# Performance work log

Measured on AMD Instinct MI355X. Metric: run time of the kernel, lower is better.

Reference implementation:

```python
import math
import jax, jax.numpy as jnp
import numpy as np

B, N, D = 4, 4096, 1024
H, M = 16, 64
HD = D // H  # 64
EPS = 1e-6


def favor_features(data, proj):
    # data: [B,H,N,hd], proj: [M,hd] -> [B,H,N,M]
    hd = data.shape[-1]
    m = proj.shape[0]
    dn = data / math.sqrt(hd)
    norm_sq = 0.5 * jnp.sum(dn * dn, axis=-1, keepdims=True)  # [B,H,N,1]
    comb = jnp.einsum('bhnd,md->bhnm', dn, proj) - norm_sq
    comb = comb - jnp.max(comb, axis=-1, keepdims=True)
    return jnp.exp(comb) / math.sqrt(m) + EPS


def setup_inputs() -> dict:
    key = jax.random.key(0)
    ks = jax.random.split(key, 6)
    x = jax.random.normal(ks[0], (B, N, D), dtype=jnp.float32)
    qkv_w = jax.random.normal(ks[1], (3 * D, D), dtype=jnp.float32) * (1.0 / math.sqrt(D))
    qkv_b = jnp.zeros((3 * D,), dtype=jnp.float32)
    proj_w = jax.random.normal(ks[2], (D, D), dtype=jnp.float32) * (1.0 / math.sqrt(D))
    proj_b = jnp.zeros((D,), dtype=jnp.float32)
    pm = jax.random.normal(ks[3], (M, HD), dtype=jnp.float32)
    pm = pm / jnp.linalg.norm(pm, axis=-1, keepdims=True)
    return {"x": x, "qkv_w": qkv_w, "qkv_b": qkv_b, "proj_w": proj_w,
            "proj_b": proj_b, "projection_matrix": pm}


def reference(x, qkv_w, qkv_b, proj_w, proj_b, projection_matrix):
    b, n, d = x.shape
    qkv = x @ qkv_w.T + qkv_b                      # [B,N,3D]
    qkv = qkv.reshape(b, n, 3, H, HD)
    qkv = jnp.transpose(qkv, (2, 0, 3, 1, 4))      # [3,B,H,N,hd]
    q, k, v = qkv[0], qkv[1], qkv[2]
    q_p = favor_features(q, projection_matrix)     # [B,H,N,M]
    k_p = favor_features(k, projection_matrix)     # [B,H,N,M]
    kv = jnp.einsum('bhnm,bhnv->bhmv', k_p, v)     # [B,H,M,hd]
    out = jnp.einsum('bhnm,bhmv->bhnv', q_p, kv)   # [B,H,N,hd]
    k_sum = jnp.sum(k_p, axis=2)                   # [B,H,M]
    normalizer = jnp.einsum('bhnm,bhm->bhn', q_p, k_sum)[..., None]
    out = out / (normalizer + EPS)
    out = jnp.transpose(out, (0, 2, 1, 3)).reshape(b, n, d)
    return out @ proj_w.T + proj_b
```

## Files before the change

kernel.cpp:

```cpp
#include <hip/hip_runtime.h>
#include <math.h>

#define B_  4
#define N_  4096
#define D_  1024
#define H_  16
#define HD_ 64
#define M_  64
#define TD_ 3072
#define EPS_ 1e-6f

typedef __attribute__((ext_vector_type(8))) short short8;
typedef __attribute__((ext_vector_type(4))) float floatx4;
typedef unsigned int uint32;

__device__ __forceinline__ void cvt2(float f0, float f1, uint32& hp, uint32& lp)
{
    uint32 b0 = __float_as_uint(f0), b1 = __float_as_uint(f1);
    hp = (b1 & 0xFFFF0000u) | (b0 >> 16);
    float l0 = f0 - __uint_as_float(b0 & 0xFFFF0000u);
    float l1 = f1 - __uint_as_float(b1 & 0xFFFF0000u);
    lp = (__float_as_uint(l1) & 0xFFFF0000u) | (__float_as_uint(l0) >> 16);
}

#define LDSTR 40

__global__ __launch_bounds__(256, 2) void gemm_bf16x2_nt_bias(
    const float* __restrict__ A, const float* __restrict__ Bm,
    const float* __restrict__ bias, float* __restrict__ C,
    int Nx, int Kx)
{
    __shared__ __align__(16) unsigned short AhiS[128*LDSTR], AloS[128*LDSTR];
    __shared__ __align__(16) unsigned short BhiS[128*LDSTR], BloS[128*LDSTR];

    const int t    = threadIdx.x;
    const int bm   = blockIdx.y * 128, bn = blockIdx.x * 128;
    const int lane = t & 63, wave = t >> 6;
    const int wm   = wave >> 1, wn = wave & 1;
    const int l16  = lane & 15, quad = lane >> 4;
    const int r    = t >> 1;
    const int ko   = (t & 1) * 16;

    floatx4 acc[4][4];
#pragma unroll
    for (int i = 0; i < 4; i++)
#pragma unroll
        for (int j = 0; j < 4; j++) acc[i][j] = (floatx4)0.f;

    const float* ap = A  + (size_t)(bm + r) * Kx + ko;
    const float* bp = Bm + (size_t)(bn + r) * Kx + ko;

    for (int k0 = 0; k0 < Kx; k0 += 32) {
        float4 fa0 = *(const float4*)(ap + k0);
        float4 fa1 = *(const float4*)(ap + k0 + 4);
        float4 fa2 = *(const float4*)(ap + k0 + 8);
        float4 fa3 = *(const float4*)(ap + k0 + 12);
        float4 fb0 = *(const float4*)(bp + k0);
        float4 fb1 = *(const float4*)(bp + k0 + 4);
        float4 fb2 = *(const float4*)(bp + k0 + 8);
        float4 fb3 = *(const float4*)(bp + k0 + 12);

        __syncthreads();

        uint4 h0, h1, l0, l1;
        cvt2(fa0.x, fa0.y, h0.x, l0.x); cvt2(fa0.z, fa0.w, h0.y, l0.y);
        cvt2(fa1.x, fa1.y, h0.z, l0.z); cvt2(fa1.z, fa1.w, h0.w, l0.w);
        cvt2(fa2.x, fa2.y, h1.x, l1.x); cvt2(fa2.z, fa2.w, h1.y, l1.y);
        cvt2(fa3.x, fa3.y, h1.z, l1.z); cvt2(fa3.z, fa3.w, h1.w, l1.w);
        *(uint4*)&AhiS[r*LDSTR + ko]     = h0;
        *(uint4*)&AhiS[r*LDSTR + ko + 8] = h1;
        *(uint4*)&AloS[r*LDSTR + ko]     = l0;
        *(uint4*)&AloS[r*LDSTR + ko + 8] = l1;

        cvt2(fb0.x, fb0.y, h0.x, l0.x); cvt2(fb0.z, fb0.w, h0.y, l0.y);
        cvt2(fb1.x, fb1.y, h0.z, l0.z); cvt2(fb1.z, fb1.w, h0.w, l0.w);
        cvt2(fb2.x, fb2.y, h1.x, l1.x); cvt2(fb2.z, fb2.w, h1.y, l1.y);
        cvt2(fb3.x, fb3.y, h1.z, l1.z); cvt2(fb3.z, fb3.w, h1.w, l1.w);
        *(uint4*)&BhiS[r*LDSTR + ko]     = h0;
        *(uint4*)&BhiS[r*LDSTR + ko + 8] = h1;
        *(uint4*)&BloS[r*LDSTR + ko]     = l0;
        *(uint4*)&BloS[r*LDSTR + ko + 8] = l1;

        __syncthreads();

        short8 ah[4], al[4], bh[4], bl[4];
#pragma unroll
        for (int mi = 0; mi < 4; mi++) {
            int row = (wm*64 + mi*16 + l16) * LDSTR + quad*8;
            ah[mi] = *(const short8*)&AhiS[row];
            al[mi] = *(const short8*)&AloS[row];
        }
#pragma unroll
        for (int ni = 0; ni < 4; ni++) {
            int row = (wn*64 + ni*16 + l16) * LDSTR + quad*8;
            bh[ni] = *(const short8*)&BhiS[row];
            bl[ni] = *(const short8*)&BloS[row];
        }
#pragma unroll
        for (int mi = 0; mi < 4; mi++)
#pragma unroll
            for (int ni = 0; ni < 4; ni++) {
                floatx4 d = acc[mi][ni];
                d = __builtin_amdgcn_mfma_f32_16x16x32_bf16(ah[mi], bh[ni], d, 0, 0, 0);
                d = __builtin_amdgcn_mfma_f32_16x16x32_bf16(al[mi], bh[ni], d, 0, 0, 0);
                d = __builtin_amdgcn_mfma_f32_16x16x32_bf16(ah[mi], bl[ni], d, 0, 0, 0);
                acc[mi][ni] = d;
            }
    }

    float bia[4];
#pragma unroll
    for (int ni = 0; ni < 4; ni++)
        bia[ni] = bias[bn + wn*64 + ni*16 + l16];
#pragma unroll
    for (int mi = 0; mi < 4; mi++)
#pragma unroll
        for (int rr = 0; rr < 4; rr++) {
            int row = bm + wm*64 + mi*16 + quad*4 + rr;
            float* crow = C + (size_t)row * Nx + bn + wn*64 + l16;
#pragma unroll
            for (int ni = 0; ni < 4; ni++)
                crow[ni*16] = acc[mi][ni][rr] + bia[ni];
        }
}

__global__ __launch_bounds__(256) void favor_features_kernel(
    const float* __restrict__ qkvb, const float* __restrict__ proj,
    float* __restrict__ qp, float* __restrict__ kp)
{
    __shared__ float  projT[64*64];
    __shared__ float4 dnbuf[4][64];
    const int t = threadIdx.x;
    const int wave = t >> 6, lane = t & 63;
    const int part = blockIdx.y;
    float* outp = (part == 0) ? qp : kp;

    for (int i = t; i < 4096; i += 256)
        projT[(i & 63) * 64 + (i >> 6)] = proj[i];
    __syncthreads();

    const int h = blockIdx.x >> 6;
    const int n0 = (blockIdx.x & 63) * 64;
    const float* src = qkvb + part * D_ + h * HD_ + lane;

    for (int iter = 0; iter < 4; iter++) {
        const int n = n0 + iter * 16 + wave * 4;
        float v0 = src[(size_t)(n+0) * TD_];
        float v1 = src[(size_t)(n+1) * TD_];
        float v2 = src[(size_t)(n+2) * TD_];
        float v3 = src[(size_t)(n+3) * TD_];
        float4 dn = make_float4(v0*0.125f, v1*0.125f, v2*0.125f, v3*0.125f);
        dnbuf[wave][lane] = dn;
        float s0 = dn.x*dn.x, s1 = dn.y*dn.y, s2 = dn.z*dn.z, s3 = dn.w*dn.w;
#pragma unroll
        for (int off = 32; off >= 1; off >>= 1) {
            s0 += __shfl_xor(s0, off, 64);
            s1 += __shfl_xor(s1, off, 64);
            s2 += __shfl_xor(s2, off, 64);
            s3 += __shfl_xor(s3, off, 64);
        }
        float c0 = -0.5f*s0, c1 = -0.5f*s1, c2 = -0.5f*s2, c3 = -0.5f*s3;
#pragma unroll
        for (int d = 0; d < 64; d++) {
            float p = projT[d*64 + lane];
            float4 q = dnbuf[wave][d];
            c0 = fmaf(q.x, p, c0);
            c1 = fmaf(q.y, p, c1);
            c2 = fmaf(q.z, p, c2);
            c3 = fmaf(q.w, p, c3);
        }
        float m0 = c0, m1 = c1, m2 = c2, m3 = c3;
#pragma unroll
        for (int off = 32; off >= 1; off >>= 1) {
            m0 = fmaxf(m0, __shfl_xor(m0, off, 64));
            m1 = fmaxf(m1, __shfl_xor(m1, off, 64));
            m2 = fmaxf(m2, __shfl_xor(m2, off, 64));
            m3 = fmaxf(m3, __shfl_xor(m3, off, 64));
        }
        float r0 = expf(c0 - m0) * 0.125f + EPS_;
        float r1 = expf(c1 - m1) * 0.125f + EPS_;
        float r2 = expf(c2 - m2) * 0.125f + EPS_;
        float r3 = expf(c3 - m3) * 0.125f + EPS_;
        size_t orow = ((size_t)h * N_ + n) * 64 + lane;
        outp[orow]       = r0;
        outp[orow + 64]  = r1;
        outp[orow + 128] = r2;
        outp[orow + 192] = r3;
    }
}

__global__ __launch_bounds__(256) void kv_partial_kernel(
    const float* __restrict__ qkvb, const float* __restrict__ kp,
    float* __restrict__ kvpart, float* __restrict__ kspart)
{
    const int t = threadIdx.x;
    const int h = blockIdx.x;
    const int c = blockIdx.y;
    const int n0 = c * 128;
    const int m0 = (t & 15) * 4;
    const int v0 = (t >> 4) * 4;

    const float* kpsrc = kp + ((size_t)h * N_ + n0) * 64 + m0;
    const float* vsrc  = qkvb + (size_t)n0 * TD_ + 2 * D_ + h * HD_ + v0;

    float acc[4][4];
#pragma unroll
    for (int i = 0; i < 4; i++)
#pragma unroll
        for (int j = 0; j < 4; j++) acc[i][j] = 0.f;
    float ks[4] = {0.f, 0.f, 0.f, 0.f};

#pragma unroll 4
    for (int n = 0; n < 128; n++) {
        float4 kq = *(const float4*)(kpsrc + (size_t)n * 64);
        float4 vq = *(const float4*)(vsrc  + (size_t)n * TD_);
        acc[0][0] = fmaf(kq.x, vq.x, acc[0][0]);
        acc[0][1] = fmaf(kq.x, vq.y, acc[0][1]);
        acc[0][2] = fmaf(kq.x, vq.z, acc[0][2]);
        acc[0][3] = fmaf(kq.x, vq.w, acc[0][3]);
        acc[1][0] = fmaf(kq.y, vq.x, acc[1][0]);
        acc[1][1] = fmaf(kq.y, vq.y, acc[1][1]);
        acc[1][2] = fmaf(kq.y, vq.z, acc[1][2]);
        acc[1][3] = fmaf(kq.y, vq.w, acc[1][3]);
        acc[2][0] = fmaf(kq.z, vq.x, acc[2][0]);
        acc[2][1] = fmaf(kq.z, vq.y, acc[2][1]);
        acc[2][2] = fmaf(kq.z, vq.z, acc[2][2]);
        acc[2][3] = fmaf(kq.z, vq.w, acc[2][3]);
        acc[3][0] = fmaf(kq.w, vq.x, acc[3][0]);
        acc[3][1] = fmaf(kq.w, vq.y, acc[3][1]);
        acc[3][2] = fmaf(kq.w, vq.z, acc[3][2]);
        acc[3][3] = fmaf(kq.w, vq.w, acc[3][3]);
        if (v0 == 0) {
            ks[0] += kq.x; ks[1] += kq.y; ks[2] += kq.z; ks[3] += kq.w;
        }
    }

    float* kvp = kvpart + (((size_t)h * 32 + c) * 4096) + m0 * 64 + v0;
#pragma unroll
    for (int i = 0; i < 4; i++)
        *(float4*)(kvp + i * 64) = make_float4(acc[i][0], acc[i][1], acc[i][2], acc[i][3]);

    if (v0 == 0) {
        float* ksp = kspart + ((size_t)h * 32 + c) * 64 + m0;
        *(float4*)ksp = make_float4(ks[0], ks[1], ks[2], ks[3]);
    }
}

__global__ __launch_bounds__(256) void kv_reduce_kernel(
    const float* __restrict__ kvpart, const float* __restrict__ kspart,
    float* __restrict__ kv, float* __restrict__ ksum)
{
    const int t = threadIdx.x;
    const int h = blockIdx.x;
    const int e0 = t * 16;

    float4 s[4];
#pragma unroll
    for (int i = 0; i < 4; i++) s[i] = make_float4(0.f, 0.f, 0.f, 0.f);
    float kss = 0.f;

    for (int c = 0; c < 32; c++) {
        const float* p = kvpart + (((size_t)h * 32 + c) * 4096) + e0;
#pragma unroll
        for (int i = 0; i < 4; i++) {
            float4 x = *(const float4*)(p + i * 4);
            s[i].x += x.x; s[i].y += x.y; s[i].z += x.z; s[i].w += x.w;
        }
        if (t < 64) kss += kspart[((size_t)h * 32 + c) * 64 + t];
    }

    float* kvo = kv + (size_t)h * 4096 + e0;
#pragma unroll
    for (int i = 0; i < 4; i++) *(float4*)(kvo + i * 4) = s[i];
    if (t < 64) ksum[h * 64 + t] = kss;
}

__global__ __launch_bounds__(256) void out_kernel(
    const float* __restrict__ qp, const float* __restrict__ kv,
    const float* __restrict__ ksum, float* __restrict__ attn)
{
    __shared__ float  kvs[4096];
    __shared__ float  kss[64];
    __shared__ float4 qbuf[4][64];
    const int t = threadIdx.x, lane = t & 63, wave = t >> 6;
    const int h = blockIdx.x;
    const int n0 = blockIdx.y * 64;

    for (int i = t; i < 4096; i += 256) kvs[i] = kv[(size_t)h * 4096 + i];
    if (t < 64) kss[t] = ksum[h * 64 + t];
    __syncthreads();

    const float* qsrc = qp + (size_t)h * N_ * 64 + lane;
    float* adst = attn + h * HD_ + lane;

    for (int iter = 0; iter < 4; iter++) {
        const int n = n0 + iter * 16 + wave * 4;
        float q0 = qsrc[(size_t)(n+0) * 64];
        float q1 = qsrc[(size_t)(n+1) * 64];
        float q2 = qsrc[(size_t)(n+2) * 64];
        float q3 = qsrc[(size_t)(n+3) * 64];
        qbuf[wave][lane] = make_float4(q0, q1, q2, q3);
        float t0 = q0 * kss[lane], t1 = q1 * kss[lane];
        float t2 = q2 * kss[lane], t3 = q3 * kss[lane];
#pragma unroll
        for (int off = 32; off >= 1; off >>= 1) {
            t0 += __shfl_xor(t0, off, 64);
            t1 += __shfl_xor(t1, off, 64);
            t2 += __shfl_xor(t2, off, 64);
            t3 += __shfl_xor(t3, off, 64);
        }
        float a0 = 0.f, a1 = 0.f, a2 = 0.f, a3 = 0.f;
#pragma unroll
        for (int m = 0; m < 64; m++) {
            float kvv = kvs[m*64 + lane];
            float4 q = qbuf[wave][m];
            a0 = fmaf(q.x, kvv, a0);
            a1 = fmaf(q.y, kvv, a1);
            a2 = fmaf(q.z, kvv, a2);
            a3 = fmaf(q.w, kvv, a3);
        }
        adst[(size_t)(n+0) * D_] = a0 / (t0 + EPS_);
        adst[(size_t)(n+1) * D_] = a1 / (t1 + EPS_);
        adst[(size_t)(n+2) * D_] = a2 / (t2 + EPS_);
        adst[(size_t)(n+3) * D_] = a3 / (t3 + EPS_);
    }
}

extern "C" void kernel_launch(void* const* d_in, const int* in_sizes, int n_in,
                              void* d_out, int out_size, void* d_ws, size_t ws_size,
                              hipStream_t stream)
{
    const float* x      = (const float*)d_in[0];
    const float* qkv_w  = (const float*)d_in[1];
    const float* qkv_b  = (const float*)d_in[2];
    const float* proj_w = (const float*)d_in[3];
    const float* proj_b = (const float*)d_in[4];
    const float* pm     = (const float*)d_in[5];
    float* out = (float*)d_out;
    float* ws  = (float*)d_ws;

    float* qkvb   = ws;
    float* qp     = ws + 12582912;
    float* kp     = qp + 4194304;
    float* kvb    = kp + 4194304;
    float* ksum   = kvb + 65536;
    float* kvpart = ksum + 1024;
    float* kspart = kvpart + 2097152;
    float* attn   = qkvb;

    for (int b = 0; b < B_; b++) {
        const float* xb = x + (size_t)b * N_ * D_;
        float* outb = out + (size_t)b * N_ * D_;

        dim3 g1(TD_ / 128, N_ / 128);
        gemm_bf16x2_nt_bias<<<g1, 256, 0, stream>>>(xb, qkv_w, qkv_b, qkvb, TD_, D_);

        dim3 g2(1024, 2);
        favor_features_kernel<<<g2, 256, 0, stream>>>(qkvb, pm, qp, kp);

        dim3 g3(16, 32);
        kv_partial_kernel<<<g3, 256, 0, stream>>>(qkvb, kp, kvpart, kspart);
        kv_reduce_kernel<<<16, 256, 0, stream>>>(kvpart, kspart, kvb, ksum);

        dim3 g4(16, 64);
        out_kernel<<<g4, 256, 0, stream>>>(qp, kvb, ksum, attn);

        dim3 g5(D_ / 128, N_ / 128);
        gemm_bf16x2_nt_bias<<<g5, 256, 0, stream>>>(attn, proj_w, proj_b, outb, D_, D_);
    }
}
```

Baseline: 1.107 ms.

## Pre-split GEMM operands into bf16 hi/lo arrays outside the GEMM loop

Adds a split kernel that converts fp32 weights and activations into separate bf16 hi and lo arrays. The GEMM now loads these directly instead of redoing the conversion inside every tile. The out kernel writes the attention output already split for the projection GEMM. The weights are split once per call and then reused across batches, which removes repeated conversion ALU work inside the GEMMs. The cost is an extra pass over x and more workspace, and the split kernel's global traffic is added while the GEMM's load volume stays the same.

```diff
diff --git a/kernel.cpp b/kernel.cpp
--- a/kernel.cpp
+++ b/kernel.cpp
@@ -13,6 +13,7 @@
 typedef __attribute__((ext_vector_type(8))) short short8;
 typedef __attribute__((ext_vector_type(4))) float floatx4;
 typedef unsigned int uint32;
+typedef unsigned short ushort;
 
 __device__ __forceinline__ void cvt2(float f0, float f1, uint32& hp, uint32& lp)
 {
@@ -23,15 +24,31 @@
     lp = (__float_as_uint(l1) & 0xFFFF0000u) | (__float_as_uint(l0) >> 16);
 }
 
+__global__ __launch_bounds__(256) void split_kernel(
+    const float* __restrict__ src, ushort* __restrict__ hi,
+    ushort* __restrict__ lo, int n)
+{
+    size_t i = ((size_t)blockIdx.x * 256 + threadIdx.x) * 8;
+    if (i >= (size_t)n) return;
+    float4 f0 = *(const float4*)(src + i);
+    float4 f1 = *(const float4*)(src + i + 4);
+    uint4 h, l;
+    cvt2(f0.x, f0.y, h.x, l.x); cvt2(f0.z, f0.w, h.y, l.y);
+    cvt2(f1.x, f1.y, h.z, l.z); cvt2(f1.z, f1.w, h.w, l.w);
+    *(uint4*)(hi + i) = h;
+    *(uint4*)(lo + i) = l;
+}
+
 #define LDSTR 40
 
-__global__ __launch_bounds__(256, 2) void gemm_bf16x2_nt_bias(
-    const float* __restrict__ A, const float* __restrict__ Bm,
+__global__ __launch_bounds__(256, 2) void gemm_presplit_nt_bias(
+    const ushort* __restrict__ Ah, const ushort* __restrict__ Al,
+    const ushort* __restrict__ Bh, const ushort* __restrict__ Bl,
     const float* __restrict__ bias, float* __restrict__ C,
     int Nx, int Kx)
 {
-    __shared__ __align__(16) unsigned short AhiS[128*LDSTR], AloS[128*LDSTR];
-    __shared__ __align__(16) unsigned short BhiS[128*LDSTR], BloS[128*LDSTR];
+    __shared__ __align__(16) ushort AhiS[128*LDSTR], AloS[128*LDSTR];
+    __shared__ __align__(16) ushort BhiS[128*LDSTR], BloS[128*LDSTR];
 
     const int t    = threadIdx.x;
     const int bm   = blockIdx.y * 128, bn = blockIdx.x * 128;
@@ -47,39 +64,31 @@
 #pragma unroll
         for (int j = 0; j < 4; j++) acc[i][j] = (floatx4)0.f;
 
-    const float* ap = A  + (size_t)(bm + r) * Kx + ko;
-    const float* bp = Bm + (size_t)(bn + r) * Kx + ko;
+    const ushort* aph = Ah + (size_t)(bm + r) * Kx + ko;
+    const ushort* apl = Al + (size_t)(bm + r) * Kx + ko;
+    const ushort* bph = Bh + (size_t)(bn + r) * Kx + ko;
+    const ushort* bpl = Bl + (size_t)(bn + r) * Kx + ko;
 
     for (int k0 = 0; k0 < Kx; k0 += 32) {
-        float4 fa0 = *(const float4*)(ap + k0);
-        float4 fa1 = *(const float4*)(ap + k0 + 4);
-        float4 fa2 = *(const float4*)(ap + k0 + 8);
-        float4 fa3 = *(const float4*)(ap + k0 + 12);
-        float4 fb0 = *(const float4*)(bp + k0);
-        float4 fb1 = *(const float4*)(bp + k0 + 4);
-        float4 fb2 = *(const float4*)(bp + k0 + 8);
-        float4 fb3 = *(const float4*)(bp + k0 + 12);
+        uint4 vah0 = *(const uint4*)(aph + k0);
+        uint4 vah1 = *(const uint4*)(aph + k0 + 8);
+        uint4 val0 = *(const uint4*)(apl + k0);
+        uint4 val1 = *(const uint4*)(apl + k0 + 8);
+        uint4 vbh0 = *(const uint4*)(bph + k0);
+        uint4 vbh1 = *(const uint4*)(bph + k0 + 8);
+        uint4 vbl0 = *(const uint4*)(bpl + k0);
+        uint4 vbl1 = *(const uint4*)(bpl + k0 + 8);
 
         __syncthreads();
 
-        uint4 h0, h1, l0, l1;
-        cvt2(fa0.x, fa0.y, h0.x, l0.x); cvt2(fa0.z, fa0.w, h0.y, l0.y);
-        cvt2(fa1.x, fa1.y, h0.z, l0.z); cvt2(fa1.z, fa1.w, h0.w, l0.w);
-        cvt2(fa2.x, fa2.y, h1.x, l1.x); cvt2(fa2.z, fa2.w, h1.y, l1.y);
-        cvt2(fa3.x, fa3.y, h1.z, l1.z); cvt2(fa3.z, fa3.w, h1.w, l1.w);
-        *(uint4*)&AhiS[r*LDSTR + ko]     = h0;
-        *(uint4*)&AhiS[r*LDSTR + ko + 8] = h1;
-        *(uint4*)&AloS[r*LDSTR + ko]     = l0;
-        *(uint4*)&AloS[r*LDSTR + ko + 8] = l1;
-
-        cvt2(fb0.x, fb0.y, h0.x, l0.x); cvt2(fb0.z, fb0.w, h0.y, l0.y);
-        cvt2(fb1.x, fb1.y, h0.z, l0.z); cvt2(fb1.z, fb1.w, h0.w, l0.w);
-        cvt2(fb2.x, fb2.y, h1.x, l1.x); cvt2(fb2.z, fb2.w, h1.y, l1.y);
-        cvt2(fb3.x, fb3.y, h1.z, l1.z); cvt2(fb3.z, fb3.w, h1.w, l1.w);
-        *(uint4*)&BhiS[r*LDSTR + ko]     = h0;
-        *(uint4*)&BhiS[r*LDSTR + ko + 8] = h1;
-        *(uint4*)&BloS[r*LDSTR + ko]     = l0;
-        *(uint4*)&BloS[r*LDSTR + ko + 8] = l1;
+        *(uint4*)&AhiS[r*LDSTR + ko]     = vah0;
+        *(uint4*)&AhiS[r*LDSTR + ko + 8] = vah1;
+        *(uint4*)&AloS[r*LDSTR + ko]     = val0;
+        *(uint4*)&AloS[r*LDSTR + ko + 8] = val1;
+        *(uint4*)&BhiS[r*LDSTR + ko]     = vbh0;
+        *(uint4*)&BhiS[r*LDSTR + ko + 8] = vbh1;
+        *(uint4*)&BloS[r*LDSTR + ko]     = vbl0;
+        *(uint4*)&BloS[r*LDSTR + ko + 8] = vbl1;
 
         __syncthreads();
 
@@ -277,7 +286,8 @@
 
 __global__ __launch_bounds__(256) void out_kernel(
     const float* __restrict__ qp, const float* __restrict__ kv,
-    const float* __restrict__ ksum, float* __restrict__ attn)
+    const float* __restrict__ ksum, ushort* __restrict__ attn_hi,
+    ushort* __restrict__ attn_lo)
 {
     __shared__ float  kvs[4096];
     __shared__ float  kss[64];
@@ -291,7 +301,7 @@
     __syncthreads();
 
     const float* qsrc = qp + (size_t)h * N_ * 64 + lane;
-    float* adst = attn + h * HD_ + lane;
+    const size_t dbase = h * HD_ + lane;
 
     for (int iter = 0; iter < 4; iter++) {
         const int n = n0 + iter * 16 + wave * 4;
@@ -319,10 +329,17 @@
             a2 = fmaf(q.z, kvv, a2);
             a3 = fmaf(q.w, kvv, a3);
         }
-        adst[(size_t)(n+0) * D_] = a0 / (t0 + EPS_);
-        adst[(size_t)(n+1) * D_] = a1 / (t1 + EPS_);
-        adst[(size_t)(n+2) * D_] = a2 / (t2 + EPS_);
-        adst[(size_t)(n+3) * D_] = a3 / (t3 + EPS_);
+        float r[4];
+        r[0] = a0 / (t0 + EPS_); r[1] = a1 / (t1 + EPS_);
+        r[2] = a2 / (t2 + EPS_); r[3] = a3 / (t3 + EPS_);
+#pragma unroll
+        for (int i = 0; i < 4; i++) {
+            uint32 bits = __float_as_uint(r[i]);
+            float lof = r[i] - __uint_as_float(bits & 0xFFFF0000u);
+            size_t idx = (size_t)(n + i) * D_ + dbase;
+            attn_hi[idx] = (ushort)(bits >> 16);
+            attn_lo[idx] = (ushort)(__float_as_uint(lof) >> 16);
+        }
     }
 }
 
@@ -340,20 +357,37 @@
     float* ws  = (float*)d_ws;
 
     float* qkvb   = ws;
-    float* qp     = ws + 12582912;
-    float* kp     = qp + 4194304;
-    float* kvb    = kp + 4194304;
+    float* qpreg  = ws + 12582912;
+    float* kpreg  = qpreg + 4194304;
+    float* kvb    = kpreg + 4194304;
     float* ksum   = kvb + 65536;
     float* kvpart = ksum + 1024;
     float* kspart = kvpart + 2097152;
-    float* attn   = qkvb;
+    float* wsplit = kspart + 32768;
+
+    ushort* xw_hi   = (ushort*)qpreg;
+    ushort* xw_lo   = xw_hi + 4194304;
+    float*  qp      = qpreg;
+    float*  kp      = kpreg;
+    ushort* attn_hi = (ushort*)kpreg;
+    ushort* attn_lo = attn_hi + 4194304;
+    ushort* qkvw_hi = (ushort*)wsplit;
+    ushort* qkvw_lo = qkvw_hi + 3145728;
+    ushort* projw_hi= qkvw_lo + 3145728;
+    ushort* projw_lo= projw_hi + 1048576;
+
+    split_kernel<<<TD_*D_/2048, 256, 0, stream>>>(qkv_w, qkvw_hi, qkvw_lo, TD_*D_);
+    split_kernel<<<D_*D_/2048,  256, 0, stream>>>(proj_w, projw_hi, projw_lo, D_*D_);
 
     for (int b = 0; b < B_; b++) {
         const float* xb = x + (size_t)b * N_ * D_;
         float* outb = out + (size_t)b * N_ * D_;
 
+        split_kernel<<<N_*D_/2048, 256, 0, stream>>>(xb, xw_hi, xw_lo, N_*D_);
+
         dim3 g1(TD_ / 128, N_ / 128);
-        gemm_bf16x2_nt_bias<<<g1, 256, 0, stream>>>(xb, qkv_w, qkv_b, qkvb, TD_, D_);
+        gemm_presplit_nt_bias<<<g1, 256, 0, stream>>>(
+            xw_hi, xw_lo, qkvw_hi, qkvw_lo, qkv_b, qkvb, TD_, D_);
 
         dim3 g2(1024, 2);
         favor_features_kernel<<<g2, 256, 0, stream>>>(qkvb, pm, qp, kp);
@@ -363,9 +397,10 @@
         kv_reduce_kernel<<<16, 256, 0, stream>>>(kvpart, kspart, kvb, ksum);
 
         dim3 g4(16, 64);
-        out_kernel<<<g4, 256, 0, stream>>>(qp, kvb, ksum, attn);
+        out_kernel<<<g4, 256, 0, stream>>>(qp, kvb, ksum, attn_hi, attn_lo);
 
         dim3 g5(D_ / 128, N_ / 128);
-        gemm_bf16x2_nt_bias<<<g5, 256, 0, stream>>>(attn, proj_w, proj_b, outb, D_, D_);
-    }
-}
+        gemm_presplit_nt_bias<<<g5, 256, 0, stream>>>(
+            attn_hi, attn_lo, projw_hi, projw_lo, proj_b, outb, D_, D_);
+    }
+}
```

Result: faster. 1.078 ms (-2.6%).
